# Optimization experiments

Hardware: AMD Instinct MI355X
Metric: run time of the kernel (lower is better)

## Reference

```python
import jax, jax.numpy as jnp
import numpy as np

B, C, L = 8, 1024, 1024
H = 16
D = C // H  # 64 samples per head
GROUPS = 32  # GroupNorm32: channels > 64 -> 32 groups
EPS = 1e-5


def setup_inputs() -> dict:
    key = jax.random.key(0)
    ks = jax.random.split(key, 5)
    x = jax.random.normal(ks[0], (B, C, L), dtype=jnp.float32)
    gn_weight = jnp.ones((C,), jnp.float32)
    gn_bias = jnp.zeros((C,), jnp.float32)
    qkv_w = jax.random.normal(ks[1], (3 * C, C), jnp.float32) * 0.02
    qkv_b = jax.random.normal(ks[2], (3 * C,), jnp.float32) * 0.02
    out_w = jax.random.normal(ks[3], (C, C), jnp.float32) * 0.02
    out_b = jax.random.normal(ks[4], (C,), jnp.float32) * 0.02
    return {"x": x, "gn_weight": gn_weight, "gn_bias": gn_bias,
            "qkv_w": qkv_w, "qkv_b": qkv_b, "out_w": out_w, "out_b": out_b,
            "qk_bias": 0}


def _group_norm(x, w, b):
    # x: [B, C, L]; normalize over (C//GROUPS, L) per group, in float32
    xg = x.astype(jnp.float32).reshape(B, GROUPS, -1)
    mu = xg.mean(axis=-1, keepdims=True)
    var = xg.var(axis=-1, keepdims=True)
    xn = ((xg - mu) * jax.lax.rsqrt(var + EPS)).reshape(B, C, L)
    return (xn * w[None, :, None] + b[None, :, None]).astype(x.dtype)


def reference(x, gn_weight, gn_bias, qkv_w, qkv_b, out_w, out_b, qk_bias):
    scale = 1.0 / np.sqrt(D).astype(np.float32)
    xn = _group_norm(x, gn_weight, gn_bias)
    # 1x1 conv == pointwise matmul over channels
    qkv = jnp.einsum('oc,bcl->bol', qkv_w, xn) + qkv_b[None, :, None]  # [B,3C,L]
    # reshape (B, H, 3D, L) and split exactly as torch .split(D, dim=2)
    qkv = qkv.reshape(B, H, 3 * D, L)
    q, k, v = qkv[:, :, :D], qkv[:, :, D:2 * D], qkv[:, :, 2 * D:]
    q = jnp.swapaxes(q, -1, -2) * scale  # [B,H,L,D]
    k = k * scale                        # [B,H,D,L]
    v = jnp.swapaxes(v, -1, -2)          # [B,H,L,D]
    score = jnp.einsum('bhld,bhdm->bhlm', q, k) + qk_bias  # [B,H,L,L]
    weights = jax.nn.softmax(score.astype(jnp.float32), axis=-1)
    ctx = jnp.einsum('bhlm,bhmd->bhld', weights, v)  # [B,H,L,D]
    ctx = jnp.swapaxes(ctx, -1, -2).reshape(B, C, L)
    h = jnp.einsum('oc,bcl->bol', out_w, ctx) + out_b[None, :, None]
    return xn + h  # residual uses the normalized x, as in the source
```

## Files before the change

### kernel.cpp

```cpp
#include <hip/hip_runtime.h>

using bf16x8 = __attribute__((ext_vector_type(8))) __bf16;
using f32x4  = __attribute__((ext_vector_type(4))) float;
using f32x16 = __attribute__((ext_vector_type(16))) float;
typedef __attribute__((ext_vector_type(2))) unsigned u32x2;
typedef __attribute__((ext_vector_type(4))) unsigned u32x4;

#define DEV __device__ __forceinline__

DEV unsigned short f2bf(float f){
  unsigned u = __builtin_bit_cast(unsigned, f);
  u += 0x7fffu + ((u >> 16) & 1u);
  return (unsigned short)(u >> 16);
}

DEV void load_lds16(const void* g, void* l){
  __builtin_amdgcn_global_load_lds((const __attribute__((address_space(1))) unsigned*)g,
                                   (__attribute__((address_space(3))) unsigned*)l, 16, 0, 0);
}

DEV f32x4 mfma16(bf16x8 a, bf16x8 b, f32x4 c){
  return __builtin_amdgcn_mfma_f32_16x16x32_bf16(a, b, c, 0, 0, 0);
}

DEV f32x16 mfma32(bf16x8 a, bf16x8 b, f32x16 c){
  return __builtin_amdgcn_mfma_f32_32x32x16_bf16(a, b, c, 0, 0, 0);
}

DEV float exp2_hw(float x){
  float r;
  asm("v_exp_f32 %0, %1" : "=v"(r) : "v"(x));
  return r;
}

DEV unsigned cvtpk_bf16(float a, float b){
  unsigned r;
  asm("v_cvt_pk_bf16_f32 %0, %1, %2" : "=v"(r) : "v"(a), "v"(b));
  return r;
}

DEV void permswap(unsigned &a, unsigned &b){
  asm volatile("v_permlane32_swap_b32 %0, %1" : "+v"(a), "+v"(b));
}

__global__ void wconv_k(const float* __restrict__ a, unsigned short* __restrict__ o, int n4){
  for (int i = blockIdx.x * blockDim.x + threadIdx.x; i < n4; i += gridDim.x * blockDim.x){
    float4 v = reinterpret_cast<const float4*>(a)[i];
    ushort4 u;
    u.x = f2bf(v.x); u.y = f2bf(v.y); u.z = f2bf(v.z); u.w = f2bf(v.w);
    reinterpret_cast<ushort4*>(o)[i] = u;
  }
}

__global__ __launch_bounds__(256) void gn_stats_k(const float* __restrict__ x, float* __restrict__ st){
  int bg = blockIdx.x;
  const float4* xp = reinterpret_cast<const float4*>(x + (size_t)bg * 32768);
  float s = 0.f, ss = 0.f;
  for (int i = threadIdx.x; i < 8192; i += 256){
    float4 v = xp[i];
    s  += (v.x + v.y) + (v.z + v.w);
    ss += (v.x*v.x + v.y*v.y) + (v.z*v.z + v.w*v.w);
  }
  #pragma unroll
  for (int off = 32; off; off >>= 1){ s += __shfl_down(s, off); ss += __shfl_down(ss, off); }
  __shared__ float rs[4], rss[4];
  if ((threadIdx.x & 63) == 0){ rs[threadIdx.x >> 6] = s; rss[threadIdx.x >> 6] = ss; }
  __syncthreads();
  if (threadIdx.x == 0){
    s  = (rs[0] + rs[1]) + (rs[2] + rs[3]);
    ss = (rss[0] + rss[1]) + (rss[2] + rss[3]);
    float mu  = s * (1.0f / 32768.0f);
    float var = ss * (1.0f / 32768.0f) - mu * mu;
    st[bg*2]   = mu;
    st[bg*2+1] = rsqrtf(var + 1e-5f);
  }
}

__global__ __launch_bounds__(256) void gn_norm_k(const float* __restrict__ x,
                                                 const float* __restrict__ gw,
                                                 const float* __restrict__ gb,
                                                 const float* __restrict__ st,
                                                 float* __restrict__ xn,
                                                 unsigned short* __restrict__ xnt){
  int t = blockIdx.x;
  int tile = t & 15; int g = (t >> 4) & 31; int bb = t >> 9;
  float mu = st[(bb*32+g)*2], rstd = st[(bb*32+g)*2+1];
  __shared__ unsigned short lt[64*32];
  int tid = threadIdx.x;
  int l = tid & 63;
  int c0 = tid >> 6;
  size_t base = ((size_t)bb*1024 + g*32) * 1024 + tile*64;
  #pragma unroll
  for (int cb = 0; cb < 8; ++cb){
    int c = cb*4 + c0;
    size_t idx = base + (size_t)c*1024 + l;
    float xv = x[idx];
    int cg = g*32 + c;
    float v = (xv - mu) * rstd * gw[cg] + gb[cg];
    xn[idx] = v;
    lt[l*32 + c] = f2bf(v);
  }
  __syncthreads();
  int lr = tid >> 2, sl = tid & 3;
  uint4 u = *reinterpret_cast<uint4*>(&lt[lr*32 + sl*8]);
  size_t ob = ((size_t)bb*1024 + tile*64 + lr) * 1024 + g*32 + sl*8;
  *reinterpret_cast<uint4*>(&xnt[ob]) = u;
}

template<int MODE>
__global__ __launch_bounds__(256) void gemm_k(const unsigned short* __restrict__ A,
                                              const unsigned short* __restrict__ Bm,
                                              const float* __restrict__ bias,
                                              float* __restrict__ outf,
                                              unsigned short* __restrict__ qo,
                                              unsigned short* __restrict__ ko,
                                              unsigned short* __restrict__ vo){
  constexpr int MT = MODE ? 8 : 24;
  constexpr int CHUNK = MT * 8;
  __shared__ char sA[16384];
  __shared__ char sB[16384];
  const int tid = threadIdx.x;
  const int w = tid >> 6, ln = tid & 63, hi = ln >> 4, lo = ln & 15;
  const int wrow = w >> 1, wcol = w & 1;
  const int bxo = (int)blockIdx.x;
  const int bx = (bxo & 7) * CHUNK + (bxo >> 3);
  const int b = bx / (MT*8);
  const int rem = bx % (MT*8);
  const int mt = rem >> 3, nt = rem & 7;
  const char* Ag = (const char*)A + (size_t)mt*128*2048;
  const char* Bg = (const char*)Bm + ((size_t)b*1024 + nt*128)*2048;
  f32x4 acc[4][4] = {};
  for (int kk = 0; kk < 16; ++kk){
    #pragma unroll
    for (int i = 0; i < 4; ++i){
      int s = tid*16 + i*4096;
      int row = s >> 7;
      int byte = (s & 127) ^ ((row & 7) << 4);
      size_t off = (size_t)row*2048 + kk*128 + byte;
      load_lds16(Ag + off, sA + s);
      load_lds16(Bg + off, sB + s);
    }
    __syncthreads();
    #pragma unroll
    for (int ks = 0; ks < 2; ++ks){
      bf16x8 af[4], bq[4];
      #pragma unroll
      for (int mi = 0; mi < 4; ++mi){
        int row = wrow*64 + mi*16 + lo;
        af[mi] = *reinterpret_cast<const bf16x8*>(sA + row*128 + ((ks*64 + hi*16) ^ ((row & 7) << 4)));
      }
      #pragma unroll
      for (int ni = 0; ni < 4; ++ni){
        int row = wcol*64 + ni*16 + lo;
        bq[ni] = *reinterpret_cast<const bf16x8*>(sB + row*128 + ((ks*64 + hi*16) ^ ((row & 7) << 4)));
      }
      #pragma unroll
      for (int mi = 0; mi < 4; ++mi)
        #pragma unroll
        for (int ni = 0; ni < 4; ++ni)
          acc[mi][ni] = mfma16(af[mi], bq[ni], acc[mi][ni]);
    }
    __syncthreads();
  }
  if (MODE == 0){
    #pragma unroll
    for (int mi = 0; mi < 4; ++mi){
      const int o0 = mt*128 + wrow*64 + mi*16 + hi*4;
      const int hh = o0 / 192;
      const int rr = o0 % 192;
      const size_t hb = (size_t)b*16 + hh;
      float bv0 = bias[o0], bv1 = bias[o0+1], bv2 = bias[o0+2], bv3 = bias[o0+3];
      #pragma unroll
      for (int ni = 0; ni < 4; ++ni){
        const int l = nt*128 + wcol*64 + ni*16 + lo;
        if (rr < 64){
          ushort4 u;
          u.x = f2bf(acc[mi][ni][0] + bv0); u.y = f2bf(acc[mi][ni][1] + bv1);
          u.z = f2bf(acc[mi][ni][2] + bv2); u.w = f2bf(acc[mi][ni][3] + bv3);
          *reinterpret_cast<ushort4*>(qo + (hb*1024 + l)*64 + rr) = u;
        } else if (rr < 128){
          ushort4 u;
          u.x = f2bf(acc[mi][ni][0] + bv0); u.y = f2bf(acc[mi][ni][1] + bv1);
          u.z = f2bf(acc[mi][ni][2] + bv2); u.w = f2bf(acc[mi][ni][3] + bv3);
          *reinterpret_cast<ushort4*>(ko + (hb*1024 + l)*64 + (rr - 64)) = u;
        } else {
          const int d = rr - 128;
          vo[(hb*64 + d + 0)*1024 + l] = f2bf(acc[mi][ni][0] + bv0);
          vo[(hb*64 + d + 1)*1024 + l] = f2bf(acc[mi][ni][1] + bv1);
          vo[(hb*64 + d + 2)*1024 + l] = f2bf(acc[mi][ni][2] + bv2);
          vo[(hb*64 + d + 3)*1024 + l] = f2bf(acc[mi][ni][3] + bv3);
        }
      }
    }
  } else {
    #pragma unroll
    for (int mi = 0; mi < 4; ++mi){
      const int o0 = mt*128 + wrow*64 + mi*16 + hi*4;
      #pragma unroll
      for (int ni = 0; ni < 4; ++ni){
        const int l = nt*128 + wcol*64 + ni*16 + lo;
        #pragma unroll
        for (int r = 0; r < 4; ++r){
          size_t idx = ((size_t)b*1024 + o0 + r) * 1024 + l;
          outf[idx] += acc[mi][ni][r] + bias[o0 + r];
        }
      }
    }
  }
}

__global__ __launch_bounds__(256) void attn_k(const unsigned short* __restrict__ qt,
                                              const unsigned short* __restrict__ kt,
                                              const unsigned short* __restrict__ vt,
                                              unsigned short* __restrict__ ctx){
  __shared__ char sK[2][8192];
  __shared__ char sV[2][8192];
  __shared__ float sRed[4][32];
  const int tid = threadIdx.x;
  const int w = tid >> 6, ln = tid & 63;
  const int hi5 = ln >> 5, lo5 = ln & 31;
  const int bxo = (int)blockIdx.x;
  const int bx = (bxo & 7) * 128 + (bxo >> 3);
  const int qb = bx & 7;
  const int bh = bx >> 3;
  const unsigned short* qp = qt + ((size_t)bh*1024 + qb*128 + w*32 + lo5) * 64;
  bf16x8 qreg[4];
  #pragma unroll
  for (int d = 0; d < 4; ++d)
    qreg[d] = *reinterpret_cast<const bf16x8*>(qp + d*16 + hi5*8);
  const char* kg = (const char*)(kt + (size_t)bh*65536);
  const char* vg = (const char*)(vt + (size_t)bh*65536);
  f32x16 oa0 = {}, oa1 = {};
  float m = 0.f, l = 0.f;

  auto STAGE = [&](int buf, int kb){
    #pragma unroll
    for (int i = 0; i < 2; ++i){
      int s = tid*16 + i*4096;
      int row = s >> 7;
      int byte = (s & 127) ^ ((row & 7) << 4);
      load_lds16(kg + (size_t)(kb*64 + row)*128 + byte, sK[buf] + s);
      load_lds16(vg + (size_t)row*2048 + kb*128 + byte, sV[buf] + s);
    }
  };

  const float sc2 = 0.015625f * 1.44269504f;

  STAGE(0, 0);
  asm volatile("s_waitcnt vmcnt(0)" ::: "memory");
  __builtin_amdgcn_s_barrier();

  for (int kb = 0; kb < 16; ++kb){
    const int cur = kb & 1;
    STAGE(cur ^ 1, (kb + 1) & 15);

    const char* kbase0 = sK[cur] + lo5*128;
    const char* kbase1 = sK[cur] + (32 + lo5)*128;
    const int ksw = (lo5 & 7) << 4;
    f32x16 s0 = {}, s1 = {};
    #pragma unroll
    for (int d = 0; d < 4; ++d){
      int off = (d*32 + hi5*16) ^ ksw;
      bf16x8 ka = *reinterpret_cast<const bf16x8*>(kbase0 + off);
      bf16x8 kb8 = *reinterpret_cast<const bf16x8*>(kbase1 + off);
      s0 = mfma32(ka, qreg[d], s0);
      s1 = mfma32(kb8, qreg[d], s1);
    }

    float t[16];
    #pragma unroll
    for (int i = 0; i < 16; ++i) t[i] = fmaxf(s0[i], s1[i]);
    #pragma unroll
    for (int st = 8; st; st >>= 1)
      #pragma unroll
      for (int i = 0; i < st; ++i) t[i] = fmaxf(t[i], t[i+st]);
    float mx = fmaxf(t[0], __shfl_xor(t[0], 32));
    float m2 = mx * sc2;

    if (__builtin_expect(__any(m2 > m + 8.f), 0)){
      float nm = fmaxf(m, m2);
      float corr = exp2_hw(m - nm);
      m = nm; l *= corr;
      sRed[w][lo5] = corr;
      __builtin_amdgcn_wave_barrier();
      #pragma unroll
      for (int r = 0; r < 16; ++r){
        float cc = sRed[w][(r & 3) + 8*(r >> 2) + 4*hi5];
        oa0[r] *= cc; oa1[r] *= cc;
      }
      __builtin_amdgcn_wave_barrier();
    }

    float ps[16];
    #pragma unroll
    for (int i = 0; i < 16; ++i){
      float p0 = exp2_hw(fmaf(s0[i], sc2, -m));
      float p1 = exp2_hw(fmaf(s1[i], sc2, -m));
      s0[i] = p0; s1[i] = p1;
      ps[i] = p0 + p1;
    }
    #pragma unroll
    for (int st = 8; st; st >>= 1)
      #pragma unroll
      for (int i = 0; i < st; ++i) ps[i] += ps[i+st];
    l += ps[0] + __shfl_xor(ps[0], 32);

    bf16x8 pa[4];
    #pragma unroll
    for (int sl = 0; sl < 4; ++sl){
      const int c0 = 2*(sl & 1), c1 = c0 + 1;
      unsigned w0, w1, w2, w3;
      if (sl < 2){
        w0 = cvtpk_bf16(s0[4*c0+0], s0[4*c0+1]);
        w1 = cvtpk_bf16(s0[4*c0+2], s0[4*c0+3]);
        w2 = cvtpk_bf16(s0[4*c1+0], s0[4*c1+1]);
        w3 = cvtpk_bf16(s0[4*c1+2], s0[4*c1+3]);
      } else {
        w0 = cvtpk_bf16(s1[4*c0+0], s1[4*c0+1]);
        w1 = cvtpk_bf16(s1[4*c0+2], s1[4*c0+3]);
        w2 = cvtpk_bf16(s1[4*c1+0], s1[4*c1+1]);
        w3 = cvtpk_bf16(s1[4*c1+2], s1[4*c1+3]);
      }
      permswap(w0, w2);
      permswap(w1, w3);
      u32x4 pc; pc.x = w0; pc.y = w1; pc.z = w2; pc.w = w3;
      pa[sl] = __builtin_bit_cast(bf16x8, pc);
    }

    const char* vb0 = sV[cur] + lo5*128;
    const char* vb1 = sV[cur] + (32 + lo5)*128;
    #pragma unroll
    for (int sl = 0; sl < 4; ++sl){
      int off = (sl*32 + hi5*16) ^ ksw;
      bf16x8 v0 = *reinterpret_cast<const bf16x8*>(vb0 + off);
      bf16x8 v1 = *reinterpret_cast<const bf16x8*>(vb1 + off);
      oa0 = mfma32(pa[sl], v0, oa0);
      oa1 = mfma32(pa[sl], v1, oa1);
    }

    asm volatile("s_waitcnt vmcnt(0)" ::: "memory");
    __builtin_amdgcn_s_barrier();
  }

  sRed[w][lo5] = l;
  __builtin_amdgcn_wave_barrier();
  const int b = bh >> 4, h = bh & 15;
  #pragma unroll
  for (int r = 0; r < 16; ++r){
    int ql = (r & 3) + 8*(r >> 2) + 4*hi5;
    float inv = __builtin_amdgcn_rcpf(sRed[w][ql]);
    size_t rowb = ((size_t)b*1024 + qb*128 + w*32 + ql) * 1024 + h*64;
    ctx[rowb + lo5]      = f2bf(oa0[r] * inv);
    ctx[rowb + 32 + lo5] = f2bf(oa1[r] * inv);
  }
}

extern "C" void kernel_launch(void* const* d_in, const int* in_sizes, int n_in,
                              void* d_out, int out_size, void* d_ws, size_t ws_size,
                              hipStream_t stream) {
  (void)in_sizes; (void)n_in; (void)out_size; (void)ws_size;
  const float* x     = (const float*)d_in[0];
  const float* gn_w  = (const float*)d_in[1];
  const float* gn_b  = (const float*)d_in[2];
  const float* qkv_w = (const float*)d_in[3];
  const float* qkv_b = (const float*)d_in[4];
  const float* out_w = (const float*)d_in[5];
  const float* out_b = (const float*)d_in[6];
  float* out = (float*)d_out;
  char* ws = (char*)d_ws;
  unsigned short* xnt  = (unsigned short*)(ws);
  unsigned short* qwb  = (unsigned short*)(ws + 16777216);
  unsigned short* owb  = (unsigned short*)(ws + 23068672);
  unsigned short* qt   = (unsigned short*)(ws + 25165824);
  unsigned short* kt   = (unsigned short*)(ws + 41943040);
  unsigned short* vs   = (unsigned short*)(ws + 58720256);
  unsigned short* ctxt = (unsigned short*)(ws + 75497472);
  float*          st   = (float*)(ws + 92274688);

  wconv_k<<<512, 256, 0, stream>>>(qkv_w, qwb, 786432);
  wconv_k<<<512, 256, 0, stream>>>(out_w, owb, 262144);
  gn_stats_k<<<256, 256, 0, stream>>>(x, st);
  gn_norm_k<<<4096, 256, 0, stream>>>(x, gn_w, gn_b, st, out, xnt);
  gemm_k<0><<<1536, 256, 0, stream>>>(qwb, xnt, qkv_b, nullptr, qt, kt, vs);
  attn_k<<<1024, 256, 0, stream>>>(qt, kt, vs, ctxt);
  gemm_k<1><<<512, 256, 0, stream>>>(owb, ctxt, out_b, out, nullptr, nullptr, nullptr);
}
```

Measured before the change: 288.1 us.

## Read K/V directly from global memory in attention, dropping LDS staging

The attention kernel no longer double-buffers K and V tiles in shared memory through async global-to-LDS loads with swizzling and per-iteration barriers. Each wave now loads its K and V fragments straight from global memory, relying on L1/L2 to serve the reuse across the four waves. This removes barrier synchronisation and LDS traffic, but gives up explicit prefetch overlap and makes every wave issue its own redundant global loads.

```diff
diff --git a/kernel.cpp b/kernel.cpp
--- a/kernel.cpp
+++ b/kernel.cpp
@@ -3,7 +3,6 @@
 using bf16x8 = __attribute__((ext_vector_type(8))) __bf16;
 using f32x4  = __attribute__((ext_vector_type(4))) float;
 using f32x16 = __attribute__((ext_vector_type(16))) float;
-typedef __attribute__((ext_vector_type(2))) unsigned u32x2;
 typedef __attribute__((ext_vector_type(4))) unsigned u32x4;
 
 #define DEV __device__ __forceinline__
@@ -213,8 +212,6 @@
                                               const unsigned short* __restrict__ kt,
                                               const unsigned short* __restrict__ vt,
                                               unsigned short* __restrict__ ctx){
-  __shared__ char sK[2][8192];
-  __shared__ char sV[2][8192];
   __shared__ float sRed[4][32];
   const int tid = threadIdx.x;
   const int w = tid >> 6, ln = tid & 63;
@@ -233,36 +230,17 @@
   f32x16 oa0 = {}, oa1 = {};
   float m = 0.f, l = 0.f;
 
-  auto STAGE = [&](int buf, int kb){
-    #pragma unroll
-    for (int i = 0; i < 2; ++i){
-      int s = tid*16 + i*4096;
-      int row = s >> 7;
-      int byte = (s & 127) ^ ((row & 7) << 4);
-      load_lds16(kg + (size_t)(kb*64 + row)*128 + byte, sK[buf] + s);
-      load_lds16(vg + (size_t)row*2048 + kb*128 + byte, sV[buf] + s);
-    }
-  };
-
   const float sc2 = 0.015625f * 1.44269504f;
 
-  STAGE(0, 0);
-  asm volatile("s_waitcnt vmcnt(0)" ::: "memory");
-  __builtin_amdgcn_s_barrier();
-
   for (int kb = 0; kb < 16; ++kb){
-    const int cur = kb & 1;
-    STAGE(cur ^ 1, (kb + 1) & 15);
-
-    const char* kbase0 = sK[cur] + lo5*128;
-    const char* kbase1 = sK[cur] + (32 + lo5)*128;
-    const int ksw = (lo5 & 7) << 4;
+    const char* kr0 = kg + (size_t)(kb*64 + lo5)*128;
+    const char* kr1 = kg + (size_t)(kb*64 + 32 + lo5)*128;
     f32x16 s0 = {}, s1 = {};
     #pragma unroll
     for (int d = 0; d < 4; ++d){
-      int off = (d*32 + hi5*16) ^ ksw;
-      bf16x8 ka = *reinterpret_cast<const bf16x8*>(kbase0 + off);
-      bf16x8 kb8 = *reinterpret_cast<const bf16x8*>(kbase1 + off);
+      int off = d*32 + hi5*16;
+      bf16x8 ka  = *reinterpret_cast<const bf16x8*>(kr0 + off);
+      bf16x8 kb8 = *reinterpret_cast<const bf16x8*>(kr1 + off);
       s0 = mfma32(ka, qreg[d], s0);
       s1 = mfma32(kb8, qreg[d], s1);
     }
@@ -327,19 +305,16 @@
       pa[sl] = __builtin_bit_cast(bf16x8, pc);
     }
 
-    const char* vb0 = sV[cur] + lo5*128;
-    const char* vb1 = sV[cur] + (32 + lo5)*128;
+    const char* vr0 = vg + (size_t)lo5*2048 + kb*128;
+    const char* vr1 = vg + (size_t)(32 + lo5)*2048 + kb*128;
     #pragma unroll
     for (int sl = 0; sl < 4; ++sl){
-      int off = (sl*32 + hi5*16) ^ ksw;
-      bf16x8 v0 = *reinterpret_cast<const bf16x8*>(vb0 + off);
-      bf16x8 v1 = *reinterpret_cast<const bf16x8*>(vb1 + off);
+      int off = sl*32 + hi5*16;
+      bf16x8 v0 = *reinterpret_cast<const bf16x8*>(vr0 + off);
+      bf16x8 v1 = *reinterpret_cast<const bf16x8*>(vr1 + off);
       oa0 = mfma32(pa[sl], v0, oa0);
       oa1 = mfma32(pa[sl], v1, oa1);
     }
-
-    asm volatile("s_waitcnt vmcnt(0)" ::: "memory");
-    __builtin_amdgcn_s_barrier();
   }
 
   sRed[w][lo5] = l;
```

Result: slower. 353.0 us (+22.5%).
